# Performance work log

Measured on AMD Instinct MI355X. Metric: run time of the kernel, lower is better.

The kernel has to match this reference:

```python
import jax, jax.numpy as jnp
import numpy as np
import math

DEPTH = 4
IN_FEATURES = 1024
LEAF_WIDTH = 256
OUT_FEATURES = 1024
BATCH = 8192
N_LEAVES = 2 ** DEPTH      # 16
N_NODES = 2 ** DEPTH - 1   # 15


def setup_inputs() -> dict:
    key = jax.random.key(0)
    ks = jax.random.split(key, 8)
    l1 = 1.0 / math.sqrt(IN_FEATURES)
    l2 = 1.0 / math.sqrt(LEAF_WIDTH)
    u = lambda k, shape, f: jax.random.uniform(k, shape, jnp.float32, -f, f)
    return {
        "x": jax.random.normal(ks[0], (BATCH, IN_FEATURES), jnp.float32),
        "node_weights": u(ks[1], (N_NODES, IN_FEATURES), l1),
        "node_biases": u(ks[2], (N_NODES, 1), l1),
        "w1s": u(ks[3], (N_LEAVES, IN_FEATURES, LEAF_WIDTH), l1),
        "b1s": u(ks[4], (N_LEAVES, LEAF_WIDTH), l1),
        "w2s": u(ks[5], (N_LEAVES, LEAF_WIDTH, OUT_FEATURES), l2),
        "b2s": u(ks[6], (N_LEAVES, OUT_FEATURES), l2),
    }


def reference(x, node_weights, node_biases, w1s, b1s, w2s, b2s):
    # Soft tree-gated routing (training_forward, soft decisions, no leak).
    B = x.shape[0]
    mixture = jnp.ones((B, N_LEAVES), dtype=x.dtype)
    for d in range(DEPTH):  # static small loop over tree depth
        plat, nxt = 2 ** d - 1, 2 ** (d + 1) - 1
        n = 2 ** d
        w = node_weights[plat:nxt]          # (n, F)
        b = node_biases[plat:nxt]           # (n, 1)
        logits = x @ w.T + b.T              # (B, n)
        be = jax.nn.sigmoid(logits)
        # interleave (1-be, be) along node axis -> (B, 2n, 1)
        mod = jnp.stack([1.0 - be, be], axis=-1).reshape(B, 2 * n, 1)
        mixture = (mixture.reshape(B, 2 * n, N_LEAVES // (2 * n)) * mod).reshape(B, N_LEAVES)
    # Per-leaf two-layer MLP, then mixture-weighted sum over leaves.
    h = jnp.einsum("bf,lfh->blh", x, w1s) + b1s[None]          # (B, L, H)
    a = jax.nn.relu(h)
    y = jnp.einsum("blh,lho->blo", a, w2s) + b2s[None]          # (B, L, O)
    return jnp.sum(y * mixture[:, :, None], axis=1)             # (B, O)
```

## Files before the change

### kernel.cpp

```cpp
#include <hip/hip_runtime.h>
#include <hip/hip_bf16.h>
#include <math.h>

#define BATCH 8192
#define INF   1024
#define LEAFW 256
#define OUTF  1024
#define NLEAF 16
#define NNODE 15
#define NTOT  4096
#define KEXT  4160

typedef __bf16 bf16;
typedef __bf16 bf16x4 __attribute__((ext_vector_type(4)));
typedef __bf16 bf16x8 __attribute__((ext_vector_type(8)));
typedef float  f32x4  __attribute__((ext_vector_type(4)));

__global__ __launch_bounds__(256) void prep_gating_kernel(
    const float* __restrict__ w1, const float* __restrict__ w2,
    const float* __restrict__ b2s, const float4* __restrict__ x4,
    const float4* __restrict__ nw4, const float* __restrict__ nb,
    bf16* __restrict__ W1T, bf16* __restrict__ W2T, float* __restrict__ mg,
    bf16* __restrict__ Aact, bf16x4* __restrict__ Xbf4) {
  __shared__ float tile[64][65];
  int b = blockIdx.x;
  int t = threadIdx.x;

  if (b < 2048) {
    const float* src;
    bf16* dst;
    int srcld, dstld, r0, c0;
    if (b < 1024) {
      int l = b >> 6, rem = b & 63;
      r0 = (rem >> 2) * 64;
      c0 = (rem & 3) * 64;
      src = w1 + (size_t)l * INF * LEAFW;
      srcld = LEAFW;
      dst = W1T + (size_t)l * LEAFW * INF;
      dstld = INF;
    } else {
      int bb = b - 1024;
      int l = bb >> 6, rem = bb & 63;
      r0 = (rem >> 4) * 64;
      c0 = (rem & 15) * 64;
      src = w2 + (size_t)l * LEAFW * OUTF;
      srcld = OUTF;
      dst = W2T + l * LEAFW;
      dstld = KEXT;
    }
    int fr = t >> 4, hc4 = (t & 15) * 4;
#pragma unroll
    for (int p = 0; p < 4; ++p) {
      float4 v = *reinterpret_cast<const float4*>(
          &src[(size_t)(r0 + fr + p * 16) * srcld + c0 + hc4]);
      tile[fr + p * 16][hc4 + 0] = v.x;
      tile[fr + p * 16][hc4 + 1] = v.y;
      tile[fr + p * 16][hc4 + 2] = v.z;
      tile[fr + p * 16][hc4 + 3] = v.w;
    }
    __syncthreads();
#pragma unroll
    for (int p = 0; p < 2; ++p) {
      int s = t + p * 256;
      int h = s >> 3, fc = (s & 7) * 8;
      bf16x8 o;
#pragma unroll
      for (int e = 0; e < 8; ++e) o[e] = (bf16)tile[fc + e][h];
      *reinterpret_cast<bf16x8*>(&dst[(size_t)(c0 + h) * dstld + r0 + fc]) = o;
    }
    return;
  }

  if (b < 2304) {
    int i = (b - 2048) * 256 + t;
    int o = i >> 6, j = i & 63;
    W2T[(size_t)o * KEXT + NTOT + j] =
        (j < NLEAF) ? (bf16)b2s[(size_t)j * OUTF + o] : (bf16)0.f;
    return;
  }

  int row  = (b - 2304) * 4 + (t >> 6);
  int lane = t & 63;
  const float4* xr4 = x4 + (size_t)row * (INF / 4);

  float p[NNODE];
#pragma unroll
  for (int j = 0; j < NNODE; ++j) p[j] = 0.f;
#pragma unroll
  for (int c = 0; c < INF / 256; ++c) {
    int idx = c * 64 + lane;
    float4 xv = xr4[idx];
#pragma unroll
    for (int j = 0; j < NNODE; ++j) {
      float4 wv = nw4[j * (INF / 4) + idx];
      p[j] += xv.x * wv.x + xv.y * wv.y + xv.z * wv.z + xv.w * wv.w;
    }
    bf16x4 o = {(bf16)xv.x, (bf16)xv.y, (bf16)xv.z, (bf16)xv.w};
    Xbf4[(size_t)row * (INF / 4) + idx] = o;
  }
#pragma unroll
  for (int j = 0; j < NNODE; ++j) {
    float v = p[j];
#pragma unroll
    for (int off = 32; off > 0; off >>= 1) v += __shfl_xor(v, off);
    p[j] = 1.f / (1.f + expf(-(v + nb[j])));
  }
  float mixv[NLEAF];
#pragma unroll
  for (int L = 0; L < NLEAF; ++L) {
    int n1 = 1 + (L >> 3), n2 = 3 + (L >> 2), n3 = 7 + (L >> 1);
    float m = ((L >> 3) & 1) ? p[0] : (1.f - p[0]);
    m *= ((L >> 2) & 1) ? p[n1] : (1.f - p[n1]);
    m *= ((L >> 1) & 1) ? p[n2] : (1.f - p[n2]);
    m *= (L & 1) ? p[n3] : (1.f - p[n3]);
    mixv[L] = m;
  }
  bf16* arow = Aact + (size_t)row * KEXT + NTOT;
  if (lane == 0) {
#pragma unroll
    for (int L = 0; L < NLEAF; ++L) {
      mg[row * NLEAF + L] = mixv[L];
      arow[L] = (bf16)mixv[L];
    }
  }
  if (lane >= 16) arow[lane] = (bf16)0.f;
}

template <int N>
__device__ __forceinline__ void wait_vmcnt() {
  asm volatile("s_waitcnt vmcnt(%0)" ::"n"(N) : "memory");
}
__device__ __forceinline__ void barrier_fence() {
  asm volatile("" ::: "memory");
  __builtin_amdgcn_s_barrier();
  asm volatile("" ::: "memory");
}

template <int EPI, int KLD, int NTN>
__global__ __launch_bounds__(512, 2) void gemm_kernel(
    const bf16* __restrict__ A, const bf16* __restrict__ BT,
    const float* __restrict__ bias, const float* __restrict__ mg,
    bf16* __restrict__ outB, float* __restrict__ outF) {
  constexpr int NT  = KLD / 64;
  constexpr int ASZ = 128 * 64;
  constexpr int BSZ = 256 * 64;
  __shared__ __align__(16) bf16 As[2 * ASZ];
  __shared__ __align__(16) bf16 Bs[2 * BSZ];

  const int t = threadIdx.x, lane = t & 63, w = t >> 6;
  const int wm = w >> 2, wn = w & 3;
  const int orig = blockIdx.x;
  const int swz  = (orig & 7) * (8 * NTN) + (orig >> 3);
  const int bm = (swz / NTN) * 128, bn = (swz % NTN) * 256;
  const int lr = t >> 3, cs = t & 7;
  const int scol = ((cs ^ (lr & 7)) << 3);

  auto stageA = [&](int kt, int buf) {
#pragma unroll
    for (int q = 0; q < 2; ++q) {
      const bf16* src = A + (size_t)(bm + q * 64 + lr) * KLD + kt * 64 + scol;
      __builtin_amdgcn_global_load_lds(
          (const __attribute__((address_space(1))) void*)src,
          (__attribute__((address_space(3))) void*)((char*)As +
                                                    buf * (ASZ * 2) +
                                                    q * 8192 + t * 16),
          16, 0, 0);
    }
  };
  auto stageB = [&](int kt, int h, int buf) {
#pragma unroll
    for (int q = 0; q < 2; ++q) {
      const bf16* src =
          BT + (size_t)(bn + h * 128 + q * 64 + lr) * KLD + kt * 64 + scol;
      __builtin_amdgcn_global_load_lds(
          (const __attribute__((address_space(1))) void*)src,
          (__attribute__((address_space(3))) void*)((char*)Bs +
                                                    buf * (BSZ * 2) +
                                                    h * 16384 + q * 8192 +
                                                    t * 16),
          16, 0, 0);
    }
  };
  auto rdA = [&](int buf, int i, int kk) -> bf16x8 {
    int r  = (i >> 1) * 64 + wm * 32 + (i & 1) * 16 + (lane & 15);
    int ch = ((kk << 2) + (lane >> 4)) ^ (lane & 7);
    return *reinterpret_cast<const bf16x8*>(
        &As[buf * ASZ + r * 64 + ch * 8]);
  };
  auto rdB = [&](int buf, int j, int kk) -> bf16x8 {
    int r  = wn * 32 + (j & 1) * 16 + (lane & 15);
    int ch = ((kk << 2) + (lane >> 4)) ^ (lane & 7);
    return *reinterpret_cast<const bf16x8*>(
        &Bs[buf * BSZ + (j >> 1) * 8192 + r * 64 + ch * 8]);
  };

  f32x4 acc[4][4];
#pragma unroll
  for (int i = 0; i < 4; ++i)
#pragma unroll
    for (int j = 0; j < 4; ++j) acc[i][j] = (f32x4){0.f, 0.f, 0.f, 0.f};

  stageA(0, 0);
  stageB(0, 0, 0);
  stageB(0, 1, 0);
  wait_vmcnt<2>();
  barrier_fence();

  for (int kt = 0; kt < NT; ++kt) {
    const int cur = kt & 1, nxt = cur ^ 1;
    const int k1 = kt + 1 < NT ? kt + 1 : NT - 1;
    bf16x8 af[4][2], bq0[2][2], bq1[2][2];

#pragma unroll
    for (int i = 0; i < 4; ++i)
#pragma unroll
      for (int kk = 0; kk < 2; ++kk) af[i][kk] = rdA(cur, i, kk);
#pragma unroll
    for (int j = 0; j < 2; ++j)
#pragma unroll
      for (int kk = 0; kk < 2; ++kk) bq0[j][kk] = rdB(cur, j, kk);
    stageA(k1, nxt);
    stageB(k1, 0, nxt);
    __builtin_amdgcn_s_setprio(1);
#pragma unroll
    for (int kk = 0; kk < 2; ++kk)
#pragma unroll
      for (int i = 0; i < 4; ++i)
#pragma unroll
        for (int j = 0; j < 2; ++j)
          acc[i][j] = __builtin_amdgcn_mfma_f32_16x16x32_bf16(
              af[i][kk], bq0[j][kk], acc[i][j], 0, 0, 0);
    __builtin_amdgcn_s_setprio(0);
    wait_vmcnt<4>();
    barrier_fence();

#pragma unroll
    for (int j = 0; j < 2; ++j)
#pragma unroll
      for (int kk = 0; kk < 2; ++kk) bq1[j][kk] = rdB(cur, 2 + j, kk);
    stageB(k1, 1, nxt);
    __builtin_amdgcn_s_setprio(1);
#pragma unroll
    for (int kk = 0; kk < 2; ++kk)
#pragma unroll
      for (int i = 0; i < 4; ++i)
#pragma unroll
        for (int j = 0; j < 2; ++j)
          acc[i][2 + j] = __builtin_amdgcn_mfma_f32_16x16x32_bf16(
              af[i][kk], bq1[j][kk], acc[i][2 + j], 0, 0, 0);
    __builtin_amdgcn_s_setprio(0);
    wait_vmcnt<2>();
    barrier_fence();
  }

#pragma unroll
  for (int i = 0; i < 4; ++i) {
    int rb = bm + (i >> 1) * 64 + wm * 32 + (i & 1) * 16 + ((lane >> 4) << 2);
#pragma unroll
    for (int rr = 0; rr < 4; ++rr) {
      const int grow = rb + rr;
      if constexpr (EPI == 0) {
        const float g = mg[grow * NLEAF + (bn >> 8)];
#pragma unroll
        for (int j = 0; j < 4; ++j) {
          const int gcol =
              bn + (j >> 1) * 128 + wn * 32 + (j & 1) * 16 + (lane & 15);
          float v = acc[i][j][rr] + bias[gcol];
          v = v > 0.f ? v : 0.f;
          outB[(size_t)grow * KEXT + gcol] = (bf16)(v * g);
        }
      } else {
#pragma unroll
        for (int j = 0; j < 4; ++j) {
          const int gcol =
              bn + (j >> 1) * 128 + wn * 32 + (j & 1) * 16 + (lane & 15);
          outF[(size_t)grow * OUTF + gcol] = acc[i][j][rr];
        }
      }
    }
  }
}

extern "C" void kernel_launch(void* const* d_in, const int* in_sizes, int n_in,
                              void* d_out, int out_size, void* d_ws,
                              size_t ws_size, hipStream_t stream) {
  const float* x   = (const float*)d_in[0];
  const float* nw  = (const float*)d_in[1];
  const float* nb  = (const float*)d_in[2];
  const float* w1s = (const float*)d_in[3];
  const float* b1s = (const float*)d_in[4];
  const float* w2s = (const float*)d_in[5];
  const float* b2s = (const float*)d_in[6];
  float* out = (float*)d_out;

  char* ws = (char*)d_ws;
  bf16*  Xbf  = (bf16*)(ws);
  bf16*  W1T  = (bf16*)(ws + 16777216);
  bf16*  W2T  = (bf16*)(ws + 25165824);
  float* mg   = (float*)(ws + 33685504);
  bf16*  Aact = (bf16*)(ws + 34209792);

  prep_gating_kernel<<<dim3(4352), 256, 0, stream>>>(
      w1s, w2s, b2s, (const float4*)x, (const float4*)nw, nb, W1T, W2T, mg,
      Aact, (bf16x4*)Xbf);

  gemm_kernel<0, INF, 16><<<dim3(1024), 512, 0, stream>>>(
      Xbf, W1T, b1s, mg, Aact, nullptr);
  gemm_kernel<1, KEXT, 4><<<dim3(256), 512, 0, stream>>>(
      Aact, W2T, nullptr, nullptr, nullptr, out);
}
```

Baseline: 274.9 us.

## Use 256x256 tiles with a four-phase pipelined schedule for the first GEMM

The first GEMM becomes its own kernel using 256x256 output tiles instead of 128x256, with 512 blocks instead of 1024. Its main loop interleaves half-tile LDS reads, async global-to-LDS staging and MFMA groups across four phases per k-step, with a double-buffered B fragment. The aim is more data reuse per loaded byte and better overlap of loads with MFMA work. In exchange the 128-entry accumulator set raises register pressure, there are more barriers per step, and 512 blocks may fill the CUs less evenly.

```diff
diff --git a/kernel.cpp b/kernel.cpp
--- a/kernel.cpp
+++ b/kernel.cpp
@@ -16,7 +16,7 @@
 typedef __bf16 bf16x8 __attribute__((ext_vector_type(8)));
 typedef float  f32x4  __attribute__((ext_vector_type(4)));
 
-__global__ __launch_bounds__(256) void prep_gating_kernel(
+__global__ __launch_bounds__(256) void prep_gk(
     const float* __restrict__ w1, const float* __restrict__ w2,
     const float* __restrict__ b2s, const float4* __restrict__ x4,
     const float4* __restrict__ nw4, const float* __restrict__ nb,
@@ -135,13 +135,176 @@
   __builtin_amdgcn_s_barrier();
   asm volatile("" ::: "memory");
 }
-
-template <int EPI, int KLD, int NTN>
-__global__ __launch_bounds__(512, 2) void gemm_kernel(
+__device__ __forceinline__ void lgkm0() {
+  asm volatile("s_waitcnt lgkmcnt(0)" ::: "memory");
+}
+
+__global__ __launch_bounds__(512, 2) void g1_mfma(
     const bf16* __restrict__ A, const bf16* __restrict__ BT,
     const float* __restrict__ bias, const float* __restrict__ mg,
-    bf16* __restrict__ outB, float* __restrict__ outF) {
-  constexpr int NT  = KLD / 64;
+    bf16* __restrict__ outB) {
+  constexpr int NT  = INF / 64;
+  constexpr int HSZ = 128 * 64;
+  __shared__ __align__(16) bf16 As[4 * HSZ];
+  __shared__ __align__(16) bf16 Bs[4 * HSZ];
+
+  const int t = threadIdx.x, lane = t & 63, w = t >> 6;
+  const int wm = w >> 2, wn = w & 3;
+  const int orig = blockIdx.x;
+  const int swz  = (orig & 7) * 64 + (orig >> 3);
+  const int bm = (swz >> 4) * 256, bn = (swz & 15) * 256;
+  const int lr = t >> 3, cs = t & 7;
+  const int scol = ((cs ^ (lr & 7)) << 3);
+
+  auto stageA = [&](int kt, int h, int buf) {
+#pragma unroll
+    for (int q = 0; q < 2; ++q) {
+      const bf16* src =
+          A + (size_t)(bm + h * 128 + q * 64 + lr) * INF + kt * 64 + scol;
+      __builtin_amdgcn_global_load_lds(
+          (const __attribute__((address_space(1))) void*)src,
+          (__attribute__((address_space(3))) void*)((char*)As +
+                                                    (buf * 2 + h) * 16384 +
+                                                    q * 8192 + t * 16),
+          16, 0, 0);
+    }
+  };
+  auto stageB = [&](int kt, int h, int buf) {
+#pragma unroll
+    for (int q = 0; q < 2; ++q) {
+      const bf16* src =
+          BT + (size_t)(bn + h * 128 + q * 64 + lr) * INF + kt * 64 + scol;
+      __builtin_amdgcn_global_load_lds(
+          (const __attribute__((address_space(1))) void*)src,
+          (__attribute__((address_space(3))) void*)((char*)Bs +
+                                                    (buf * 2 + h) * 16384 +
+                                                    q * 8192 + t * 16),
+          16, 0, 0);
+    }
+  };
+  auto rdAh = [&](int buf, int h, bf16x8 (&d)[4][2]) {
+#pragma unroll
+    for (int i = 0; i < 4; ++i)
+#pragma unroll
+      for (int kk = 0; kk < 2; ++kk) {
+        int r  = wm * 64 + i * 16 + (lane & 15);
+        int ch = ((kk << 2) + (lane >> 4)) ^ (lane & 7);
+        d[i][kk] = *reinterpret_cast<const bf16x8*>(
+            &As[(buf * 2 + h) * HSZ + r * 64 + ch * 8]);
+      }
+  };
+  auto rdBh = [&](int buf, int h, bf16x8 (&d)[2][2]) {
+#pragma unroll
+    for (int j = 0; j < 2; ++j)
+#pragma unroll
+      for (int kk = 0; kk < 2; ++kk) {
+        int r  = wn * 32 + j * 16 + (lane & 15);
+        int ch = ((kk << 2) + (lane >> 4)) ^ (lane & 7);
+        d[j][kk] = *reinterpret_cast<const bf16x8*>(
+            &Bs[(buf * 2 + h) * HSZ + r * 64 + ch * 8]);
+      }
+  };
+
+  f32x4 acc[8][4];
+#pragma unroll
+  for (int i = 0; i < 8; ++i)
+#pragma unroll
+    for (int j = 0; j < 4; ++j) acc[i][j] = (f32x4){0.f, 0.f, 0.f, 0.f};
+
+  bf16x8 af0[4][2], af1[4][2], bq1[2][2], bq0a[2][2], bq0b[2][2];
+
+  stageA(0, 0, 0);
+  stageB(0, 0, 0);
+  stageB(0, 1, 0);
+  stageA(0, 1, 0);
+  stageA(1, 0, 1);
+  stageB(1, 0, 1);
+  wait_vmcnt<4>();
+  barrier_fence();
+  rdAh(0, 0, af0);
+  rdBh(0, 0, bq0a);
+
+#define MFMA16(AF, BQ, IOFF, JOFF)                                          \
+  __builtin_amdgcn_s_setprio(1);                                            \
+  _Pragma("unroll") for (int kk = 0; kk < 2; ++kk) {                        \
+    _Pragma("unroll") for (int i = 0; i < 4; ++i) {                         \
+      _Pragma("unroll") for (int j = 0; j < 2; ++j) {                       \
+        acc[(IOFF) + i][(JOFF) + j] =                                       \
+            __builtin_amdgcn_mfma_f32_16x16x32_bf16(                        \
+                AF[i][kk], BQ[j][kk], acc[(IOFF) + i][(JOFF) + j], 0, 0, 0);\
+      }                                                                     \
+    }                                                                       \
+  }                                                                         \
+  __builtin_amdgcn_s_setprio(0);
+
+#define TILE_STEP(T, CUR, BQ0C, BQ0N)                                       \
+  {                                                                         \
+    const int cur = (CUR), nxt = cur ^ 1;                                   \
+    const int tp1 = ((T) + 1 < NT) ? (T) + 1 : NT - 1;                      \
+    const int tp2 = ((T) + 2 < NT) ? (T) + 2 : NT - 1;                      \
+                        \
+    rdBh(cur, 1, bq1);                                                      \
+    stageB(tp1, 1, nxt);                                                    \
+    barrier_fence();                                                        \
+    lgkm0();                                                                \
+    MFMA16(af0, BQ0C, 0, 0);                                                \
+    barrier_fence();                                                        \
+              \
+    rdAh(cur, 1, af1);                                                      \
+    stageA(tp1, 1, nxt);                                                    \
+    barrier_fence();                                                        \
+    lgkm0();                                                                \
+    MFMA16(af0, bq1, 0, 2);                                                 \
+    wait_vmcnt<4>();                                                        \
+    barrier_fence();                                                        \
+                      \
+    rdAh(nxt, 0, af0);                                                      \
+    stageA(tp2, 0, cur);                                                    \
+    barrier_fence();                                                        \
+    lgkm0();                                                                \
+    MFMA16(af1, bq1, 4, 2);                                                 \
+    barrier_fence();                                                        \
+            \
+    rdBh(nxt, 0, BQ0N);                                                     \
+    stageB(tp2, 0, cur);                                                    \
+    barrier_fence();                                                        \
+    lgkm0();                                                                \
+    MFMA16(af1, BQ0C, 4, 0);                                                \
+    wait_vmcnt<4>();                                                        \
+    barrier_fence();                                                        \
+  }
+
+  for (int kt = 0; kt < NT; kt += 2) {
+    TILE_STEP(kt, 0, bq0a, bq0b);
+    TILE_STEP(kt + 1, 1, bq0b, bq0a);
+  }
+#undef TILE_STEP
+#undef MFMA16
+
+  const int leaf = bn >> 8;
+#pragma unroll
+  for (int i = 0; i < 8; ++i) {
+    int rb = bm + (i >> 2) * 128 + wm * 64 + (i & 3) * 16 + ((lane >> 4) << 2);
+#pragma unroll
+    for (int rr = 0; rr < 4; ++rr) {
+      const int grow = rb + rr;
+      const float g  = mg[grow * NLEAF + leaf];
+#pragma unroll
+      for (int j = 0; j < 4; ++j) {
+        const int gcol =
+            bn + (j >> 1) * 128 + wn * 32 + (j & 1) * 16 + (lane & 15);
+        float v = acc[i][j][rr] + bias[gcol];
+        v = v > 0.f ? v : 0.f;
+        outB[(size_t)grow * KEXT + gcol] = (bf16)(v * g);
+      }
+    }
+  }
+}
+
+__global__ __launch_bounds__(512, 2) void g2_mfma(
+    const bf16* __restrict__ A, const bf16* __restrict__ BT,
+    float* __restrict__ outF) {
+  constexpr int NT  = KEXT / 64;
   constexpr int ASZ = 128 * 64;
   constexpr int BSZ = 256 * 64;
   __shared__ __align__(16) bf16 As[2 * ASZ];
@@ -150,15 +313,15 @@
   const int t = threadIdx.x, lane = t & 63, w = t >> 6;
   const int wm = w >> 2, wn = w & 3;
   const int orig = blockIdx.x;
-  const int swz  = (orig & 7) * (8 * NTN) + (orig >> 3);
-  const int bm = (swz / NTN) * 128, bn = (swz % NTN) * 256;
+  const int swz  = (orig & 7) * 32 + (orig >> 3);
+  const int bm = (swz >> 2) * 128, bn = (swz & 3) * 256;
   const int lr = t >> 3, cs = t & 7;
   const int scol = ((cs ^ (lr & 7)) << 3);
 
   auto stageA = [&](int kt, int buf) {
 #pragma unroll
     for (int q = 0; q < 2; ++q) {
-      const bf16* src = A + (size_t)(bm + q * 64 + lr) * KLD + kt * 64 + scol;
+      const bf16* src = A + (size_t)(bm + q * 64 + lr) * KEXT + kt * 64 + scol;
       __builtin_amdgcn_global_load_lds(
           (const __attribute__((address_space(1))) void*)src,
           (__attribute__((address_space(3))) void*)((char*)As +
@@ -171,7 +334,7 @@
 #pragma unroll
     for (int q = 0; q < 2; ++q) {
       const bf16* src =
-          BT + (size_t)(bn + h * 128 + q * 64 + lr) * KLD + kt * 64 + scol;
+          BT + (size_t)(bn + h * 128 + q * 64 + lr) * KEXT + kt * 64 + scol;
       __builtin_amdgcn_global_load_lds(
           (const __attribute__((address_space(1))) void*)src,
           (__attribute__((address_space(3))) void*)((char*)Bs +
@@ -184,8 +347,7 @@
   auto rdA = [&](int buf, int i, int kk) -> bf16x8 {
     int r  = (i >> 1) * 64 + wm * 32 + (i & 1) * 16 + (lane & 15);
     int ch = ((kk << 2) + (lane >> 4)) ^ (lane & 7);
-    return *reinterpret_cast<const bf16x8*>(
-        &As[buf * ASZ + r * 64 + ch * 8]);
+    return *reinterpret_cast<const bf16x8*>(&As[buf * ASZ + r * 64 + ch * 8]);
   };
   auto rdB = [&](int buf, int j, int kk) -> bf16x8 {
     int r  = wn * 32 + (j & 1) * 16 + (lane & 15);
@@ -259,23 +421,11 @@
 #pragma unroll
     for (int rr = 0; rr < 4; ++rr) {
       const int grow = rb + rr;
-      if constexpr (EPI == 0) {
-        const float g = mg[grow * NLEAF + (bn >> 8)];
-#pragma unroll
-        for (int j = 0; j < 4; ++j) {
-          const int gcol =
-              bn + (j >> 1) * 128 + wn * 32 + (j & 1) * 16 + (lane & 15);
-          float v = acc[i][j][rr] + bias[gcol];
-          v = v > 0.f ? v : 0.f;
-          outB[(size_t)grow * KEXT + gcol] = (bf16)(v * g);
-        }
-      } else {
-#pragma unroll
-        for (int j = 0; j < 4; ++j) {
-          const int gcol =
-              bn + (j >> 1) * 128 + wn * 32 + (j & 1) * 16 + (lane & 15);
-          outF[(size_t)grow * OUTF + gcol] = acc[i][j][rr];
-        }
+#pragma unroll
+      for (int j = 0; j < 4; ++j) {
+        const int gcol =
+            bn + (j >> 1) * 128 + wn * 32 + (j & 1) * 16 + (lane & 15);
+        outF[(size_t)grow * OUTF + gcol] = acc[i][j][rr];
       }
     }
   }
@@ -300,12 +450,10 @@
   float* mg   = (float*)(ws + 33685504);
   bf16*  Aact = (bf16*)(ws + 34209792);
 
-  prep_gating_kernel<<<dim3(4352), 256, 0, stream>>>(
+  prep_gk<<<dim3(4352), 256, 0, stream>>>(
       w1s, w2s, b2s, (const float4*)x, (const float4*)nw, nb, W1T, W2T, mg,
       Aact, (bf16x4*)Xbf);
 
-  gemm_kernel<0, INF, 16><<<dim3(1024), 512, 0, stream>>>(
-      Xbf, W1T, b1s, mg, Aact, nullptr);
-  gemm_kernel<1, KEXT, 4><<<dim3(256), 512, 0, stream>>>(
-      Aact, W2T, nullptr, nullptr, nullptr, out);
-}
+  g1_mfma<<<dim3(512), 512, 0, stream>>>(Xbf, W1T, b1s, mg, Aact);
+  g2_mfma<<<dim3(256), 512, 0, stream>>>(Aact, W2T, out);
+}
```

After: 285.7 us. 1.04x slower.

## Triple-buffer GEMM LDS pipeline with two-stage prefetch and XCD-aware tile mapping

Applied to the files above, without the earlier changes.

Both GEMMs move from double to triple buffering in LDS. Global-to-LDS loads are now issued two k-tiles ahead, with the vmcnt waits adjusted to match, to hide more memory latency behind MFMA work. The block-to-tile mapping is also changed so blocks on the same XCD share A row panels, aiming for better L2 reuse. LDS use rises to about 144KB per block, which leaves less room for other resident blocks.

```diff
diff --git a/kernel.cpp b/kernel.cpp
--- a/kernel.cpp
+++ b/kernel.cpp
@@ -16,7 +16,7 @@
 typedef __bf16 bf16x8 __attribute__((ext_vector_type(8)));
 typedef float  f32x4  __attribute__((ext_vector_type(4)));
 
-__global__ __launch_bounds__(256) void prep_gating_kernel(
+__global__ __launch_bounds__(256) void prep_gk(
     const float* __restrict__ w1, const float* __restrict__ w2,
     const float* __restrict__ b2s, const float4* __restrict__ x4,
     const float4* __restrict__ nw4, const float* __restrict__ nb,
@@ -136,22 +136,30 @@
   asm volatile("" ::: "memory");
 }
 
-template <int EPI, int KLD, int NTN>
-__global__ __launch_bounds__(512, 2) void gemm_kernel(
+template <int EPI, int KLD, int MAP>
+__global__ __launch_bounds__(512, 2) void gemm_tb(
     const bf16* __restrict__ A, const bf16* __restrict__ BT,
     const float* __restrict__ bias, const float* __restrict__ mg,
     bf16* __restrict__ outB, float* __restrict__ outF) {
   constexpr int NT  = KLD / 64;
   constexpr int ASZ = 128 * 64;
   constexpr int BSZ = 256 * 64;
-  __shared__ __align__(16) bf16 As[2 * ASZ];
-  __shared__ __align__(16) bf16 Bs[2 * BSZ];
+  __shared__ __align__(16) bf16 As[3 * ASZ];
+  __shared__ __align__(16) bf16 Bs[3 * BSZ];
 
   const int t = threadIdx.x, lane = t & 63, w = t >> 6;
   const int wm = w >> 2, wn = w & 3;
   const int orig = blockIdx.x;
-  const int swz  = (orig & 7) * (8 * NTN) + (orig >> 3);
-  const int bm = (swz / NTN) * 128, bn = (swz % NTN) * 256;
+  int bm, bn;
+  if constexpr (MAP == 0) {
+    const int xcd = orig & 7, idx = orig >> 3;
+    bm = ((xcd << 3) + (idx & 7)) * 128;
+    bn = (idx >> 3) * 256;
+  } else {
+    const int swz = (orig & 7) * 32 + (orig >> 3);
+    bm = (swz >> 2) * 128;
+    bn = (swz & 3) * 256;
+  }
   const int lr = t >> 3, cs = t & 7;
   const int scol = ((cs ^ (lr & 7)) << 3);
 
@@ -161,8 +169,7 @@
       const bf16* src = A + (size_t)(bm + q * 64 + lr) * KLD + kt * 64 + scol;
       __builtin_amdgcn_global_load_lds(
           (const __attribute__((address_space(1))) void*)src,
-          (__attribute__((address_space(3))) void*)((char*)As +
-                                                    buf * (ASZ * 2) +
+          (__attribute__((address_space(3))) void*)((char*)As + buf * 16384 +
                                                     q * 8192 + t * 16),
           16, 0, 0);
     }
@@ -174,8 +181,7 @@
           BT + (size_t)(bn + h * 128 + q * 64 + lr) * KLD + kt * 64 + scol;
       __builtin_amdgcn_global_load_lds(
           (const __attribute__((address_space(1))) void*)src,
-          (__attribute__((address_space(3))) void*)((char*)Bs +
-                                                    buf * (BSZ * 2) +
+          (__attribute__((address_space(3))) void*)((char*)Bs + buf * 32768 +
                                                     h * 16384 + q * 8192 +
                                                     t * 16),
           16, 0, 0);
@@ -184,8 +190,7 @@
   auto rdA = [&](int buf, int i, int kk) -> bf16x8 {
     int r  = (i >> 1) * 64 + wm * 32 + (i & 1) * 16 + (lane & 15);
     int ch = ((kk << 2) + (lane >> 4)) ^ (lane & 7);
-    return *reinterpret_cast<const bf16x8*>(
-        &As[buf * ASZ + r * 64 + ch * 8]);
+    return *reinterpret_cast<const bf16x8*>(&As[buf * ASZ + r * 64 + ch * 8]);
   };
   auto rdB = [&](int buf, int j, int kk) -> bf16x8 {
     int r  = wn * 32 + (j & 1) * 16 + (lane & 15);
@@ -203,12 +208,16 @@
   stageA(0, 0);
   stageB(0, 0, 0);
   stageB(0, 1, 0);
-  wait_vmcnt<2>();
+  const int k1p = NT > 1 ? 1 : 0;
+  stageA(k1p, 1);
+  stageB(k1p, 0, 1);
+  stageB(k1p, 1, 1);
+  wait_vmcnt<8>();
   barrier_fence();
 
+  int cur = 0, stg = 2;
   for (int kt = 0; kt < NT; ++kt) {
-    const int cur = kt & 1, nxt = cur ^ 1;
-    const int k1 = kt + 1 < NT ? kt + 1 : NT - 1;
+    const int k2 = kt + 2 < NT ? kt + 2 : NT - 1;
     bf16x8 af[4][2], bq0[2][2], bq1[2][2];
 
 #pragma unroll
@@ -219,8 +228,8 @@
     for (int j = 0; j < 2; ++j)
 #pragma unroll
       for (int kk = 0; kk < 2; ++kk) bq0[j][kk] = rdB(cur, j, kk);
-    stageA(k1, nxt);
-    stageB(k1, 0, nxt);
+    stageA(k2, stg);
+    stageB(k2, 0, stg);
     __builtin_amdgcn_s_setprio(1);
 #pragma unroll
     for (int kk = 0; kk < 2; ++kk)
@@ -231,14 +240,14 @@
           acc[i][j] = __builtin_amdgcn_mfma_f32_16x16x32_bf16(
               af[i][kk], bq0[j][kk], acc[i][j], 0, 0, 0);
     __builtin_amdgcn_s_setprio(0);
-    wait_vmcnt<4>();
+    wait_vmcnt<10>();
     barrier_fence();
 
 #pragma unroll
     for (int j = 0; j < 2; ++j)
 #pragma unroll
       for (int kk = 0; kk < 2; ++kk) bq1[j][kk] = rdB(cur, 2 + j, kk);
-    stageB(k1, 1, nxt);
+    stageB(k2, 1, stg);
     __builtin_amdgcn_s_setprio(1);
 #pragma unroll
     for (int kk = 0; kk < 2; ++kk)
@@ -249,8 +258,11 @@
           acc[i][2 + j] = __builtin_amdgcn_mfma_f32_16x16x32_bf16(
               af[i][kk], bq1[j][kk], acc[i][2 + j], 0, 0, 0);
     __builtin_amdgcn_s_setprio(0);
-    wait_vmcnt<2>();
+    wait_vmcnt<8>();
     barrier_fence();
+
+    cur = cur == 2 ? 0 : cur + 1;
+    stg = stg == 2 ? 0 : stg + 1;
   }
 
 #pragma unroll
@@ -300,12 +312,12 @@
   float* mg   = (float*)(ws + 33685504);
   bf16*  Aact = (bf16*)(ws + 34209792);
 
-  prep_gating_kernel<<<dim3(4352), 256, 0, stream>>>(
+  prep_gk<<<dim3(4352), 256, 0, stream>>>(
       w1s, w2s, b2s, (const float4*)x, (const float4*)nw, nb, W1T, W2T, mg,
       Aact, (bf16x4*)Xbf);
 
-  gemm_kernel<0, INF, 16><<<dim3(1024), 512, 0, stream>>>(
+  gemm_tb<0, INF, 0><<<dim3(1024), 512, 0, stream>>>(
       Xbf, W1T, b1s, mg, Aact, nullptr);
-  gemm_kernel<1, KEXT, 4><<<dim3(256), 512, 0, stream>>>(
+  gemm_tb<1, KEXT, 1><<<dim3(256), 512, 0, stream>>>(
       Aact, W2T, nullptr, nullptr, nullptr, out);
 }
```

Result: no change. 271.7 us (-1.2%).
